# Performance work log

Measured on AMD Instinct MI355X. Metric: run time of the kernel, lower is better.

Reference implementation:

```python
import jax, jax.numpy as jnp
import numpy as np


def _pairwise_sq_dist(x, y):
    # x: [B, N, 3], y: [B, M, 3] -> P: [B, N, M] squared Euclidean distances
    xx = jnp.sum(x * x, axis=-1)                      # [B, N]
    yy = jnp.sum(y * y, axis=-1)                      # [B, M]
    zz = jnp.einsum('bnd,bmd->bnm', x, y)             # [B, N, M]
    return xx[:, :, None] + yy[:, None, :] - 2.0 * zz


def setup_inputs() -> dict:
    key = jax.random.key(0)
    k1, k2 = jax.random.split(key)
    B, K = 8, 8192
    adv_pc = jax.random.normal(k1, (B, K, 3), dtype=jnp.float32)
    ori_pc = jax.random.normal(k2, (B, K, 3), dtype=jnp.float32)
    weights = jnp.ones((B,), dtype=jnp.float32)
    return {"adv_pc": adv_pc, "ori_pc": ori_pc, "weights": weights}


def reference(adv_pc, ori_pc, weights):
    # P = pairwise_dist(gts=ori_pc, preds=adv_pc): [B, N_ori, N_adv]
    P = _pairwise_sq_dist(ori_pc, adv_pc)
    # method='adv2ori': loss1 = max over adv points of min over ori points
    loss1 = jnp.max(jnp.min(P, axis=1), axis=1)       # [B]
    loss = loss1 * weights
    return jnp.mean(loss)                             # batch_avg=True
```

## Files before the change

kernel.cpp:

```cpp
#include <hip/hip_runtime.h>


#define KPTS 8192
#define BATCH 8

#define CBLK 256
#define NSPLIT 8
#define RBLK (KPTS / NSPLIT)
#define CHUNK 512
#define NCHUNK (RBLK / CHUNK)
#define CTILES (CHUNK / 32)

typedef _Float16 half8 __attribute__((ext_vector_type(8)));
typedef float f32x16 __attribute__((ext_vector_type(16)));

__device__ __forceinline__ float min16(const f32x16 c) {
    float u0 = fminf(fminf(c[0],  c[1]),  c[2]);
    float u1 = fminf(fminf(c[3],  c[4]),  c[5]);
    float u2 = fminf(fminf(c[6],  c[7]),  c[8]);
    float u3 = fminf(fminf(c[9],  c[10]), c[11]);
    float u4 = fminf(fminf(c[12], c[13]), c[14]);
    float u5 = fminf(fminf(u0, u1), c[15]);
    float u6 = fminf(fminf(u2, u3), u4);
    return fminf(u5, u6);
}

__global__ __launch_bounds__(256) void hausdorff(const float* __restrict__ adv,
                                                 const float* __restrict__ ori,
                                                 unsigned int* __restrict__ ws,
                                                 float* __restrict__ out) {
    __shared__ _Float16 sA[CHUNK * 16];

    const int bid  = blockIdx.x;
    const int b    = bid >> 8;
    const int mc   = (bid >> 3) & 31;
    const int ns   = bid & 7;
    const int tid  = threadIdx.x;
    const int lane = tid & 63;
    const int wv   = tid >> 6;
    const int r    = lane & 31;
    const int hk   = lane >> 5;

    if (bid == 0 && tid == 0) out[0] = 0.0f;

    const _Float16 Z = (_Float16)0.0f, ONE = (_Float16)1.0f;

    const float* advb = adv + (size_t)b * KPTS * 3;
    const int m0 = mc * CBLK + wv * 64 + r;
    const int m1 = m0 + 32;
    half8 bf0, bf1;
    float aa0, aa1;
    {
        float ax = advb[3 * m0], ay = advb[3 * m0 + 1], az = advb[3 * m0 + 2];
        aa0 = ax * ax + ay * ay + az * az;
        float tx = -2.f * ax, ty = -2.f * ay, tz = -2.f * az;
        _Float16 bx = (_Float16)tx, by = (_Float16)ty, bz = (_Float16)tz;
        _Float16 cx = (_Float16)(tx - (float)bx);
        _Float16 cy = (_Float16)(ty - (float)by);
        _Float16 cz = (_Float16)(tz - (float)bz);
        half8 h0 = {bx, by, bz, cx, cy, cz, bx, by};
        half8 h1 = {bz, ONE, ONE, Z, Z, Z, Z, Z};
        bf0 = hk ? h1 : h0;
    }
    {
        float ax = advb[3 * m1], ay = advb[3 * m1 + 1], az = advb[3 * m1 + 2];
        aa1 = ax * ax + ay * ay + az * az;
        float tx = -2.f * ax, ty = -2.f * ay, tz = -2.f * az;
        _Float16 bx = (_Float16)tx, by = (_Float16)ty, bz = (_Float16)tz;
        _Float16 cx = (_Float16)(tx - (float)bx);
        _Float16 cy = (_Float16)(ty - (float)by);
        _Float16 cz = (_Float16)(tz - (float)bz);
        half8 h0 = {bx, by, bz, cx, cy, cz, bx, by};
        half8 h1 = {bz, ONE, ONE, Z, Z, Z, Z, Z};
        bf1 = hk ? h1 : h0;
    }

    f32x16 zc;
#pragma unroll
    for (int i = 0; i < 16; ++i) zc[i] = 0.0f;

    float rm0 = __builtin_huge_valf();
    float rm1 = __builtin_huge_valf();

    const float* orib = ori + (size_t)b * KPTS * 3;
    const _Float16* apl = sA + r * 16 + hk * 8;

    for (int ch = 0; ch < NCHUNK; ++ch) {
        const int rowbase = ns * RBLK + ch * CHUNK;

        __syncthreads();
        for (int rr = tid; rr < CHUNK; rr += 256) {
            const float* op = orib + (size_t)(rowbase + rr) * 3;
            float x = op[0], y = op[1], z = op[2];
            float oo = x * x + y * y + z * z;
            _Float16 hx = (_Float16)x, hy = (_Float16)y, hz = (_Float16)z;
            _Float16 lx = (_Float16)(x - (float)hx);
            _Float16 ly = (_Float16)(y - (float)hy);
            _Float16 lz = (_Float16)(z - (float)hz);
            _Float16 oh = (_Float16)oo;
            _Float16 ol = (_Float16)(oo - (float)oh);
            half8 a0 = {hx, hy, hz, hx, hy, hz, lx, ly};
            half8 a1 = {lz, oh, ol, Z, Z, Z, Z, Z};
            *(half8*)(sA + rr * 16)     = a0;
            *(half8*)(sA + rr * 16 + 8) = a1;
        }
        __syncthreads();

#pragma unroll 4
        for (int t = 0; t < CTILES; ++t) {
            half8 af = *(const half8*)(apl + (size_t)t * (32 * 16));
            f32x16 c0 = __builtin_amdgcn_mfma_f32_32x32x16_f16(af, bf0, zc, 0, 0, 0);
            f32x16 c1 = __builtin_amdgcn_mfma_f32_32x32x16_f16(af, bf1, zc, 0, 0, 0);
            rm0 = fminf(rm0, min16(c0));
            rm1 = fminf(rm1, min16(c1));
        }
    }

    rm0 = fminf(rm0, __shfl_xor(rm0, 32, 64));
    rm1 = fminf(rm1, __shfl_xor(rm1, 32, 64));

    float v0 = fmaxf(rm0 + aa0, 0.0f);
    float v1 = fmaxf(rm1 + aa1, 0.0f);

    unsigned int* wsb = ws + (size_t)b * KPTS;
    if (hk == 0) {
        unsigned int u0 = __float_as_uint(v0);
        if (u0 < wsb[m0]) atomicMin(wsb + m0, u0);
        unsigned int u1 = __float_as_uint(v1);
        if (u1 < wsb[m1]) atomicMin(wsb + m1, u1);
    }
}

__global__ __launch_bounds__(1024) void reduceB(const unsigned int* __restrict__ ws,
                                                const float* __restrict__ w,
                                                float* __restrict__ out) {
    const int b = blockIdx.x;
    const int tid = threadIdx.x;

    float mx = 0.0f;
#pragma unroll
    for (int m = tid; m < KPTS; m += 1024)
        mx = fmaxf(mx, __uint_as_float(ws[(size_t)b * KPTS + m]));

#pragma unroll
    for (int off = 32; off; off >>= 1)
        mx = fmaxf(mx, __shfl_down(mx, off, 64));

    __shared__ float red[16];
    if ((tid & 63) == 0) red[tid >> 6] = mx;
    __syncthreads();
    if (tid == 0) {
        float m2 = red[0];
#pragma unroll
        for (int i = 1; i < 16; ++i) m2 = fmaxf(m2, red[i]);
        atomicAdd(out, m2 * w[b] * (1.0f / BATCH));
    }
}

extern "C" void kernel_launch(void* const* d_in, const int* in_sizes, int n_in,
                              void* d_out, int out_size, void* d_ws, size_t ws_size,
                              hipStream_t stream) {
    const float* adv = (const float*)d_in[0];
    const float* ori = (const float*)d_in[1];
    const float* w   = (const float*)d_in[2];
    float* out = (float*)d_out;
    unsigned int* ws = (unsigned int*)d_ws;

    hipMemsetAsync(ws, 0xFF, (size_t)BATCH * KPTS * sizeof(unsigned int), stream);
    hausdorff<<<BATCH * 32 * NSPLIT, 256, 0, stream>>>(adv, ori, ws, out);
    reduceB<<<BATCH, 1024, 0, stream>>>((const unsigned int*)ws, w, out);
}
```

Measured before the change: 86.27 us.

## Double-buffer LDS staging and replace atomicMin workspace with per-split partial buffers

Ori-point staging is now double-buffered in shared memory with a smaller chunk. The next chunk's global loads are issued before the MFMA loop, and conversion and stores happen after it, so load latency overlaps compute. The memset plus atomicMin scheme is replaced by plain stores into per-split partial arrays, and the reduce kernel takes the min across the splits itself. This removes the memset launch and the atomics at the cost of a larger workspace, more reduce-side reads, and an extra barrier per chunk.

```diff
diff --git a/kernel.cpp b/kernel.cpp
--- a/kernel.cpp
+++ b/kernel.cpp
@@ -7,7 +7,7 @@
 #define CBLK 256
 #define NSPLIT 8
 #define RBLK (KPTS / NSPLIT)
-#define CHUNK 512
+#define CHUNK 256
 #define NCHUNK (RBLK / CHUNK)
 #define CTILES (CHUNK / 32)
 
@@ -27,9 +27,9 @@
 
 __global__ __launch_bounds__(256) void hausdorff(const float* __restrict__ adv,
                                                  const float* __restrict__ ori,
-                                                 unsigned int* __restrict__ ws,
+                                                 float* __restrict__ part,
                                                  float* __restrict__ out) {
-    __shared__ _Float16 sA[CHUNK * 16];
+    __shared__ _Float16 sA[2][CHUNK * 16];
 
     const int bid  = blockIdx.x;
     const int b    = bid >> 8;
@@ -83,29 +83,35 @@
     float rm1 = __builtin_huge_valf();
 
     const float* orib = ori + (size_t)b * KPTS * 3;
-    const _Float16* apl = sA + r * 16 + hk * 8;
+    const int rowbase = ns * RBLK;
+
+    float px, py, pz;
+    {
+        const float* op = orib + (size_t)(rowbase + tid) * 3;
+        px = op[0]; py = op[1]; pz = op[2];
+        float oo = px * px + py * py + pz * pz;
+        _Float16 hx = (_Float16)px, hy = (_Float16)py, hz = (_Float16)pz;
+        _Float16 lx = (_Float16)(px - (float)hx);
+        _Float16 ly = (_Float16)(py - (float)hy);
+        _Float16 lz = (_Float16)(pz - (float)hz);
+        _Float16 oh = (_Float16)oo;
+        _Float16 ol = (_Float16)(oo - (float)oh);
+        half8 a0 = {hx, hy, hz, hx, hy, hz, lx, ly};
+        half8 a1 = {lz, oh, ol, Z, Z, Z, Z, Z};
+        *(half8*)(&sA[0][tid * 16])     = a0;
+        *(half8*)(&sA[0][tid * 16 + 8]) = a1;
+    }
+    __syncthreads();
 
     for (int ch = 0; ch < NCHUNK; ++ch) {
-        const int rowbase = ns * RBLK + ch * CHUNK;
+        const int cur = ch & 1;
 
-        __syncthreads();
-        for (int rr = tid; rr < CHUNK; rr += 256) {
-            const float* op = orib + (size_t)(rowbase + rr) * 3;
-            float x = op[0], y = op[1], z = op[2];
-            float oo = x * x + y * y + z * z;
-            _Float16 hx = (_Float16)x, hy = (_Float16)y, hz = (_Float16)z;
-            _Float16 lx = (_Float16)(x - (float)hx);
-            _Float16 ly = (_Float16)(y - (float)hy);
-            _Float16 lz = (_Float16)(z - (float)hz);
-            _Float16 oh = (_Float16)oo;
-            _Float16 ol = (_Float16)(oo - (float)oh);
-            half8 a0 = {hx, hy, hz, hx, hy, hz, lx, ly};
-            half8 a1 = {lz, oh, ol, Z, Z, Z, Z, Z};
-            *(half8*)(sA + rr * 16)     = a0;
-            *(half8*)(sA + rr * 16 + 8) = a1;
+        if (ch + 1 < NCHUNK) {
+            const float* op = orib + (size_t)(rowbase + (ch + 1) * CHUNK + tid) * 3;
+            px = op[0]; py = op[1]; pz = op[2];
         }
-        __syncthreads();
 
+        const _Float16* apl = &sA[cur][r * 16 + hk * 8];
 #pragma unroll 4
         for (int t = 0; t < CTILES; ++t) {
             half8 af = *(const half8*)(apl + (size_t)t * (32 * 16));
@@ -113,6 +119,22 @@
             f32x16 c1 = __builtin_amdgcn_mfma_f32_32x32x16_f16(af, bf1, zc, 0, 0, 0);
             rm0 = fminf(rm0, min16(c0));
             rm1 = fminf(rm1, min16(c1));
+        }
+        __syncthreads();
+
+        if (ch + 1 < NCHUNK) {
+            float oo = px * px + py * py + pz * pz;
+            _Float16 hx = (_Float16)px, hy = (_Float16)py, hz = (_Float16)pz;
+            _Float16 lx = (_Float16)(px - (float)hx);
+            _Float16 ly = (_Float16)(py - (float)hy);
+            _Float16 lz = (_Float16)(pz - (float)hz);
+            _Float16 oh = (_Float16)oo;
+            _Float16 ol = (_Float16)(oo - (float)oh);
+            half8 a0 = {hx, hy, hz, hx, hy, hz, lx, ly};
+            half8 a1 = {lz, oh, ol, Z, Z, Z, Z, Z};
+            *(half8*)(&sA[cur ^ 1][tid * 16])     = a0;
+            *(half8*)(&sA[cur ^ 1][tid * 16 + 8]) = a1;
+            __syncthreads();
         }
     }
 
@@ -122,37 +144,37 @@
     float v0 = fmaxf(rm0 + aa0, 0.0f);
     float v1 = fmaxf(rm1 + aa1, 0.0f);
 
-    unsigned int* wsb = ws + (size_t)b * KPTS;
+    float* p = part + ((size_t)ns * BATCH + b) * KPTS;
     if (hk == 0) {
-        unsigned int u0 = __float_as_uint(v0);
-        if (u0 < wsb[m0]) atomicMin(wsb + m0, u0);
-        unsigned int u1 = __float_as_uint(v1);
-        if (u1 < wsb[m1]) atomicMin(wsb + m1, u1);
+        p[m0] = v0;
+        p[m1] = v1;
     }
 }
 
-__global__ __launch_bounds__(1024) void reduceB(const unsigned int* __restrict__ ws,
-                                                const float* __restrict__ w,
-                                                float* __restrict__ out) {
+__global__ __launch_bounds__(256) void reduceB(const float* __restrict__ part,
+                                               const float* __restrict__ w,
+                                               float* __restrict__ out) {
     const int b = blockIdx.x;
     const int tid = threadIdx.x;
 
     float mx = 0.0f;
+    for (int m = tid; m < KPTS; m += 256) {
+        float mn = part[(size_t)b * KPTS + m];
 #pragma unroll
-    for (int m = tid; m < KPTS; m += 1024)
-        mx = fmaxf(mx, __uint_as_float(ws[(size_t)b * KPTS + m]));
+        for (int s = 1; s < NSPLIT; ++s)
+            mn = fminf(mn, part[((size_t)s * BATCH + b) * KPTS + m]);
+        mx = fmaxf(mx, mn);
+    }
 
 #pragma unroll
     for (int off = 32; off; off >>= 1)
-        mx = fmaxf(mx, __shfl_down(mx, off, 64));
+        mx = fmaxf(mx, __shfl_xor(mx, off, 64));
 
-    __shared__ float red[16];
+    __shared__ float red[4];
     if ((tid & 63) == 0) red[tid >> 6] = mx;
     __syncthreads();
     if (tid == 0) {
-        float m2 = red[0];
-#pragma unroll
-        for (int i = 1; i < 16; ++i) m2 = fmaxf(m2, red[i]);
+        float m2 = fmaxf(fmaxf(red[0], red[1]), fmaxf(red[2], red[3]));
         atomicAdd(out, m2 * w[b] * (1.0f / BATCH));
     }
 }
@@ -164,9 +186,8 @@
     const float* ori = (const float*)d_in[1];
     const float* w   = (const float*)d_in[2];
     float* out = (float*)d_out;
-    unsigned int* ws = (unsigned int*)d_ws;
+    float* part = (float*)d_ws;
 
-    hipMemsetAsync(ws, 0xFF, (size_t)BATCH * KPTS * sizeof(unsigned int), stream);
-    hausdorff<<<BATCH * 32 * NSPLIT, 256, 0, stream>>>(adv, ori, ws, out);
-    reduceB<<<BATCH, 1024, 0, stream>>>((const unsigned int*)ws, w, out);
+    hausdorff<<<BATCH * 32 * NSPLIT, 256, 0, stream>>>(adv, ori, part, out);
+    reduceB<<<BATCH, 256, 0, stream>>>((const float*)part, w, out);
 }
```

Measured after the change: 90.11 us. 4.5% more time.
